# Optimization experiments

Hardware: AMD Instinct MI355X
Metric: run time of the kernel (lower is better)

Reference implementation:

```python
import jax, jax.numpy as jnp
import numpy as np

B, S, D, H, FF = 4, 2048, 512, 8, 2048
W = 128  # local attention window size (hardcoded in module)
DH = D // H


def _ln(x, g, b, eps=1e-5):
    m = x.mean(-1, keepdims=True)
    v = ((x - m) ** 2).mean(-1, keepdims=True)
    return (x - m) / jnp.sqrt(v + eps) * g + b


def setup_inputs() -> dict:
    key = jax.random.key(0)
    ks = jax.random.split(key, 10)
    s = 0.02
    return {
        "src": jax.random.normal(ks[0], (B, S, D), jnp.float32),
        # global nn.MultiheadAttention params
        "in_proj_w": jax.random.normal(ks[1], (3 * D, D), jnp.float32) * s,
        "in_proj_b": jnp.zeros((3 * D,), jnp.float32),
        "out_proj_w": jax.random.normal(ks[2], (D, D), jnp.float32) * s,
        "out_proj_b": jnp.zeros((D,), jnp.float32),
        # LocalMHA params (prenorm LN, fused qkv no-bias, out proj no-bias)
        "ln_g": jnp.ones((D,), jnp.float32),
        "ln_b": jnp.zeros((D,), jnp.float32),
        "qkv_w": jax.random.normal(ks[3], (3 * D, D), jnp.float32) * s,
        "to_out_w": jax.random.normal(ks[4], (D, D), jnp.float32) * s,
        # glFusion + FFN + norms
        "gl_w": jax.random.normal(ks[5], (D, 2 * D), jnp.float32) * s,
        "gl_b": jnp.zeros((D,), jnp.float32),
        "norm1_g": jnp.ones((D,), jnp.float32),
        "norm1_b": jnp.zeros((D,), jnp.float32),
        "lin1_w": jax.random.normal(ks[6], (FF, D), jnp.float32) * s,
        "lin1_b": jnp.zeros((FF,), jnp.float32),
        "lin2_w": jax.random.normal(ks[7], (D, FF), jnp.float32) * s,
        "lin2_b": jnp.zeros((D,), jnp.float32),
        "norm2_g": jnp.ones((D,), jnp.float32),
        "norm2_b": jnp.zeros((D,), jnp.float32),
    }


def _forward(src, in_proj_w, in_proj_b, out_proj_w, out_proj_b, ln_g, ln_b,
             qkv_w, to_out_w, gl_w, gl_b, norm1_g, norm1_b,
             lin1_w, lin1_b, lin2_w, lin2_b, norm2_g, norm2_b):
    b, s, d = src.shape
    scale = DH ** -0.5

    def heads(x):  # (b, s, d) -> (b, H, s, DH)
        return x.reshape(b, s, H, DH).transpose(0, 2, 1, 3)

    # ---- global full MHA (no mask) ----
    qkv = src @ in_proj_w.T + in_proj_b
    qg, kg, vg = (heads(t) for t in jnp.split(qkv, 3, axis=-1))
    att = jax.nn.softmax(jnp.einsum('bhid,bhjd->bhij', qg, kg) * scale, axis=-1)
    go = jnp.einsum('bhij,bhjd->bhid', att, vg).transpose(0, 2, 1, 3).reshape(b, s, d)
    go = go @ out_proj_w.T + out_proj_b

    # ---- local windowed causal MHA with rotary (window=128, look_backward=1) ----
    x = _ln(src, ln_g, ln_b)  # prenorm
    ql, kl, vl = (heads(t) for t in jnp.split(x @ qkv_w.T, 3, axis=-1))

    pos = jnp.arange(s)
    inv_freq = 1.0 / (10000.0 ** (jnp.arange(0, DH, 2, dtype=jnp.float32) / DH))
    freqs = pos[:, None].astype(jnp.float32) * inv_freq[None, :]
    emb = jnp.concatenate([freqs, freqs], axis=-1)  # (s, DH)
    cos, sin = jnp.cos(emb), jnp.sin(emb)

    def rope(t):
        h = DH // 2
        t1, t2 = t[..., :h], t[..., h:]
        return t * cos + jnp.concatenate([-t2, t1], axis=-1) * sin

    ql, kl = rope(ql), rope(kl)
    ql = ql * scale

    nw = s // W
    qw = ql.reshape(b, H, nw, W, DH)
    kw = kl.reshape(b, H, nw, W, DH)
    vw = vl.reshape(b, H, nw, W, DH)

    def look_back(t):  # concat previous window with current: (b,H,nw,2W,DH)
        prev = jnp.pad(t, ((0, 0), (0, 0), (1, 0), (0, 0), (0, 0)))[:, :, :-1]
        return jnp.concatenate([prev, t], axis=3)

    bk, bv = look_back(kw), look_back(vw)

    qpos = pos.reshape(nw, W)
    kpos = jnp.concatenate(
        [jnp.concatenate([jnp.full((1, W), -1, pos.dtype), qpos[:-1]], axis=0), qpos],
        axis=1)  # (nw, 2W)
    mask = (kpos[:, None, :] >= 0) & (kpos[:, None, :] <= qpos[:, :, None])  # (nw,W,2W)

    sc = jnp.einsum('bhnid,bhnjd->bhnij', qw, bk)
    sc = jnp.where(mask, sc, jnp.finfo(sc.dtype).min)
    at = jax.nn.softmax(sc, axis=-1)
    lo = jnp.einsum('bhnij,bhnjd->bhnid', at, bv).reshape(b, H, s, DH)
    lo = lo.transpose(0, 2, 1, 3).reshape(b, s, d) @ to_out_w.T

    # ---- fuse global+local, residual, norms, FFN ----
    src2 = jnp.concatenate([go, lo], axis=-1) @ gl_w.T + gl_b
    h1 = _ln(src + src2, norm1_g, norm1_b)
    ff = jax.nn.relu(h1 @ lin1_w.T + lin1_b) @ lin2_w.T + lin2_b
    return _ln(h1 + ff, norm2_g, norm2_b)


def reference(src, in_proj_w, in_proj_b, out_proj_w, out_proj_b, ln_g, ln_b,
              qkv_w, to_out_w, gl_w, gl_b, norm1_g, norm1_b,
              lin1_w, lin1_b, lin2_w, lin2_b, norm2_g, norm2_b):
    return _forward(src, in_proj_w, in_proj_b, out_proj_w, out_proj_b, ln_g, ln_b,
                    qkv_w, to_out_w, gl_w, gl_b, norm1_g, norm1_b,
                    lin1_w, lin1_b, lin2_w, lin2_b, norm2_g, norm2_b)
```

## Files before the change

kernel.cpp:

```cpp
#include <hip/hip_runtime.h>
#include <math.h>

#define B_  4
#define S_  2048
#define D_  512
#define H_  8
#define FF_ 2048
#define W_  128
#define DH_ 64
#define TRD (3*D_)
#define MR_ (B_*S_)
#define QKLD 1024
#define SCQ 0.18033688011112042f

typedef __attribute__((ext_vector_type(8)))  short short8;
typedef __attribute__((ext_vector_type(4)))  float f32x4;
typedef __attribute__((ext_vector_type(16))) float f32x16;

__device__ __forceinline__ short f2bf(float f) {
    unsigned u = __float_as_uint(f);
    unsigned r = (u + 0x7fff + ((u >> 16) & 1)) >> 16;
    return (short)r;
}
__device__ __forceinline__ float bf2f(ushort u) {
    return __uint_as_float(((unsigned)u) << 16);
}
__device__ __forceinline__ unsigned pack_bf_trunc(float f0, float f1) {
    return __builtin_amdgcn_perm(__float_as_uint(f1), __float_as_uint(f0), 0x07060302u);
}
__device__ __forceinline__ void gload_lds16(const ushort* g, short* l) {
    __builtin_amdgcn_global_load_lds(
        (const __attribute__((address_space(1))) void*)g,
        (__attribute__((address_space(3))) void*)l, 16, 0, 0);
}

struct CvtJobs { const float* s[8]; ushort* d[8]; int n[8]; };

__global__ __launch_bounds__(256) void cvt_kernel(CvtJobs jobs)
{
    int i4 = (blockIdx.x * 256 + threadIdx.x) * 4;
    #pragma unroll
    for (int j = 0; j < 8; j++) {
        if (i4 < jobs.n[j]) {
            float4 v = *(const float4*)(jobs.s[j] + i4);
            ushort4 o;
            o.x = (ushort)f2bf(v.x); o.y = (ushort)f2bf(v.y);
            o.z = (ushort)f2bf(v.z); o.w = (ushort)f2bf(v.w);
            *(ushort4*)(jobs.d[j] + i4) = o;
        }
    }
}

__global__ __launch_bounds__(256) void gemm_bf16_kernel(
    const ushort* __restrict__ A, int lda,
    const ushort* __restrict__ Wt,
    const float* __restrict__ bias,
    ushort* __restrict__ C, int ldc,
    ushort* __restrict__ vt,
    int K, int relu)
{
    __shared__ short As[128 * 64];
    __shared__ short Bs[128 * 64];
    const int tid  = threadIdx.x;
    const int w    = tid >> 6;
    const int lane = tid & 63;
    const int quad = lane >> 4;
    const int x    = lane & 15;
    const int wr = w >> 1, wc = w & 1;
    const int bm = blockIdx.y * 128;
    const int bn = blockIdx.x * 128;

    const int srow = w * 32 + (lane >> 3);
    const int scol = ((lane & 7) ^ (lane >> 3)) * 8;

    f32x4 acc[4][4];
    #pragma unroll
    for (int i = 0; i < 4; i++)
        #pragma unroll
        for (int j = 0; j < 4; j++) acc[i][j] = (f32x4)0.f;

    for (int k0 = 0; k0 < K; k0 += 64) {
        __syncthreads();
        #pragma unroll
        for (int c = 0; c < 4; c++) {
            const ushort* ga = A + (size_t)(bm + srow + c * 8) * lda + k0 + scol;
            gload_lds16(ga, &As[(w * 32 + c * 8) * 64]);
            const ushort* gb = Wt + (size_t)(bn + srow + c * 8) * K + k0 + scol;
            gload_lds16(gb, &Bs[(w * 32 + c * 8) * 64]);
        }
        __syncthreads();

        #pragma unroll
        for (int kc = 0; kc < 2; kc++) {
            short8 af[4], bf[4];
            int pcg = (kc * 4 + quad) ^ (x & 7);
            #pragma unroll
            for (int i = 0; i < 4; i++)
                af[i] = *(const short8*)&As[(wr * 64 + i * 16 + x) * 64 + pcg * 8];
            #pragma unroll
            for (int j = 0; j < 4; j++)
                bf[j] = *(const short8*)&Bs[(wc * 64 + j * 16 + x) * 64 + pcg * 8];
            #pragma unroll
            for (int i = 0; i < 4; i++)
                #pragma unroll
                for (int j = 0; j < 4; j++)
                    acc[i][j] = __builtin_amdgcn_mfma_f32_16x16x32_bf16(af[i], bf[j], acc[i][j], 0, 0, 0);
        }
    }

    if (vt) {
        #pragma unroll
        for (int i = 0; i < 4; i++) {
            int rowbase = bm + wr * 64 + i * 16 + quad * 4;
            #pragma unroll
            for (int j = 0; j < 4; j++) {
                int col = bn + wc * 64 + j * 16 + x;
                float bv = bias ? bias[col] : 0.f;
                if (col < 1024) {
                    #pragma unroll
                    for (int r = 0; r < 4; r++)
                        C[(size_t)(rowbase + r) * QKLD + col] = (ushort)f2bf(acc[i][j][r] + bv);
                } else {
                    int cv = col - 1024, hh = cv >> 6, dd = cv & 63;
                    int bb = rowbase >> 11, ss = rowbase & 2047;
                    int quadp = ((quad & 1) << 1) | (quad >> 1);
                    int sp = (ss & ~15) | (quadp << 2);
                    ushort4 p4;
                    p4.x = (ushort)f2bf(acc[i][j][0] + bv);
                    p4.y = (ushort)f2bf(acc[i][j][1] + bv);
                    p4.z = (ushort)f2bf(acc[i][j][2] + bv);
                    p4.w = (ushort)f2bf(acc[i][j][3] + bv);
                    *(ushort4*)(vt + ((size_t)((bb * 8 + hh) * 64 + dd)) * S_ + sp) = p4;
                }
            }
        }
    } else {
        #pragma unroll
        for (int i = 0; i < 4; i++) {
            #pragma unroll
            for (int r = 0; r < 4; r++) {
                size_t row = (size_t)(bm + wr * 64 + i * 16 + quad * 4 + r);
                #pragma unroll
                for (int j = 0; j < 4; j++) {
                    int col = bn + wc * 64 + j * 16 + x;
                    float v = acc[i][j][r] + (bias ? bias[col] : 0.f);
                    if (relu) v = v > 0.f ? v : 0.f;
                    C[row * ldc + col] = (ushort)f2bf(v);
                }
            }
        }
    }
}

__global__ __launch_bounds__(256) void gemm_bf16_splitk_kernel(
    const ushort* __restrict__ A, int lda,
    const ushort* __restrict__ Wt,
    float* __restrict__ P, int K)
{
    __shared__ short As[128 * 64];
    __shared__ short Bs[128 * 64];
    const int tid  = threadIdx.x;
    const int w    = tid >> 6;
    const int lane = tid & 63;
    const int quad = lane >> 4;
    const int x    = lane & 15;
    const int wr = w >> 1, wc = w & 1;
    const int bm = blockIdx.y * 128;
    const int bn = blockIdx.x * 128;
    const int kh = K >> 1;
    const int kbeg = blockIdx.z * kh;
    float* dst = P + (size_t)blockIdx.z * MR_ * D_;

    const int srow = w * 32 + (lane >> 3);
    const int scol = ((lane & 7) ^ (lane >> 3)) * 8;

    f32x4 acc[4][4];
    #pragma unroll
    for (int i = 0; i < 4; i++)
        #pragma unroll
        for (int j = 0; j < 4; j++) acc[i][j] = (f32x4)0.f;

    for (int k0 = kbeg; k0 < kbeg + kh; k0 += 64) {
        __syncthreads();
        #pragma unroll
        for (int c = 0; c < 4; c++) {
            const ushort* ga = A + (size_t)(bm + srow + c * 8) * lda + k0 + scol;
            gload_lds16(ga, &As[(w * 32 + c * 8) * 64]);
            const ushort* gb = Wt + (size_t)(bn + srow + c * 8) * K + k0 + scol;
            gload_lds16(gb, &Bs[(w * 32 + c * 8) * 64]);
        }
        __syncthreads();

        #pragma unroll
        for (int kc = 0; kc < 2; kc++) {
            short8 af[4], bf[4];
            int pcg = (kc * 4 + quad) ^ (x & 7);
            #pragma unroll
            for (int i = 0; i < 4; i++)
                af[i] = *(const short8*)&As[(wr * 64 + i * 16 + x) * 64 + pcg * 8];
            #pragma unroll
            for (int j = 0; j < 4; j++)
                bf[j] = *(const short8*)&Bs[(wc * 64 + j * 16 + x) * 64 + pcg * 8];
            #pragma unroll
            for (int i = 0; i < 4; i++)
                #pragma unroll
                for (int j = 0; j < 4; j++)
                    acc[i][j] = __builtin_amdgcn_mfma_f32_16x16x32_bf16(af[i], bf[j], acc[i][j], 0, 0, 0);
        }
    }

    #pragma unroll
    for (int i = 0; i < 4; i++)
        #pragma unroll
        for (int r = 0; r < 4; r++) {
            size_t row = (size_t)(bm + wr * 64 + i * 16 + quad * 4 + r);
            #pragma unroll
            for (int j = 0; j < 4; j++) {
                int col = bn + wc * 64 + j * 16 + x;
                dst[row * D_ + col] = acc[i][j][r];
            }
        }
}

__device__ __forceinline__ float wave_sum64(float v) {
    #pragma unroll
    for (int off = 32; off > 0; off >>= 1) v += __shfl_xor(v, off, 64);
    return v;
}
__device__ __forceinline__ void load8(const float* p, float* v) {
    *(float4*)&v[0] = *(const float4*)p;
    *(float4*)&v[4] = *(const float4*)(p + 4);
}
__device__ __forceinline__ void load8(const ushort* p, float* v) {
    short8 s = *(const short8*)p;
    #pragma unroll
    for (int i = 0; i < 8; i++) v[i] = bf2f((ushort)s[i]);
}
__device__ __forceinline__ void store8(float* p, const float* v) {
    *(float4*)p       = make_float4(v[0], v[1], v[2], v[3]);
    *(float4*)(p + 4) = make_float4(v[4], v[5], v[6], v[7]);
}
__device__ __forceinline__ void store8(ushort* p, const float* v) {
    short8 s;
    #pragma unroll
    for (int i = 0; i < 8; i++) s[i] = f2bf(v[i]);
    *(short8*)p = s;
}
__device__ __forceinline__ void ln_core(float* v, int lane,
    const float* g, const float* be, float* t) {
    float s = 0.f;
    #pragma unroll
    for (int i = 0; i < 8; i++) s += v[i];
    float mean = wave_sum64(s) * (1.0f / 512.0f);
    float vs = 0.f;
    #pragma unroll
    for (int i = 0; i < 8; i++) { float d = v[i] - mean; vs += d * d; }
    float var = wave_sum64(vs) * (1.0f / 512.0f);
    float r = rsqrtf(var + 1e-5f);
    const int c = lane * 8;
    #pragma unroll
    for (int i = 0; i < 8; i++) t[i] = (v[i] - mean) * r * g[c + i] + be[c + i];
}

template <typename TA, typename TO>
__global__ __launch_bounds__(256) void addln_kernel(
    const TA* __restrict__ a,
    const float* __restrict__ g, const float* __restrict__ be,
    TO* __restrict__ out)
{
    const int lane = threadIdx.x & 63;
    const int row  = blockIdx.x * 4 + (threadIdx.x >> 6);
    const size_t base = (size_t)row * D_ + lane * 8;
    float v[8], t[8];
    load8(a + base, v);
    ln_core(v, lane, g, be, t);
    store8(out + base, t);
}

template <typename TA, typename TO>
__global__ __launch_bounds__(256) void ln_split_kernel(
    const TA* __restrict__ a,
    const float* __restrict__ p0, const float* __restrict__ p1,
    const float* __restrict__ bias,
    const float* __restrict__ g, const float* __restrict__ be,
    TO* __restrict__ out)
{
    const int lane = threadIdx.x & 63;
    const int row  = blockIdx.x * 4 + (threadIdx.x >> 6);
    const size_t base = (size_t)row * D_ + lane * 8;
    float v[8], w0[8], w1[8], t[8];
    load8(a + base, v);
    load8(p0 + base, w0);
    load8(p1 + base, w1);
    const int c = lane * 8;
    #pragma unroll
    for (int i = 0; i < 8; i++) v[i] += w0[i] + w1[i] + bias[c + i];
    ln_core(v, lane, g, be, t);
    store8(out + base, t);
}

__global__ __launch_bounds__(256) void transpose512_kernel(
    const ushort* __restrict__ in, ushort* __restrict__ out)
{
    __shared__ ushort T[64][72];
    const int t  = threadIdx.x;
    const int r0 = blockIdx.y * 64, c0 = blockIdx.x * 64;
    {
        int row = t >> 2, col = (t & 3) * 16;
        const ushort* s = in + (size_t)(r0 + row) * 512 + c0 + col;
        *(short8*)&T[row][col]     = *(const short8*)s;
        *(short8*)&T[row][col + 8] = *(const short8*)(s + 8);
    }
    __syncthreads();
    {
        int d = t >> 2, sc = (t & 3) * 16;
        ushort tmp[16];
        #pragma unroll
        for (int k = 0; k < 16; k++) tmp[k] = T[sc + k][d];
        ushort* dptr = out + (size_t)(c0 + d) * 512 + r0 + sc;
        *(short8*)dptr       = *(const short8*)&tmp[0];
        *(short8*)(dptr + 8) = *(const short8*)&tmp[8];
    }
}

__global__ __launch_bounds__(256) void fuse_bias_kernel(
    const float* __restrict__ gl_w, const float* __restrict__ opb,
    const float* __restrict__ gl_b, float* __restrict__ bf)
{
    const int lane = threadIdx.x & 63;
    const int row  = blockIdx.x * 4 + (threadIdx.x >> 6);
    float s = 0.f;
    #pragma unroll
    for (int i = 0; i < 8; i++) {
        int m = lane * 8 + i;
        s += gl_w[(size_t)row * 1024 + m] * opb[m];
    }
    s = wave_sum64(s);
    if (lane == 0) bf[row] = s + gl_b[row];
}

__global__ __launch_bounds__(256) void rope_kernel(ushort* __restrict__ qk)
{
    int idx = blockIdx.x * 256 + threadIdx.x;
    int d8 = idx & 3;
    int h  = (idx >> 2) & 7;
    int bs = idx >> 5;
    int pos = bs & (S_ - 1);
    ushort* base = qk + (size_t)bs * QKLD + h * 64 + d8 * 8;
    float q1[8], q2[8], k1[8], k2[8];
    load8(base, q1);       load8(base + 32, q2);
    load8(base + 512, k1); load8(base + 544, k2);
    float oq1[8], oq2[8], ok1[8], ok2[8];
    #pragma unroll
    for (int i = 0; i < 8; i++) {
        int d = d8 * 8 + i;
        float inv_freq = exp2f(-(float)d * (2.0f / 64.0f) * 13.287712379549449f);
        float ang = (float)pos * inv_freq;
        float sn, cs;
        __sincosf(ang, &sn, &cs);
        oq1[i] = (q1[i] * cs - q2[i] * sn) * SCQ;
        oq2[i] = (q2[i] * cs + q1[i] * sn) * SCQ;
        ok1[i] = k1[i] * cs - k2[i] * sn;
        ok2[i] = k2[i] * cs + k1[i] * sn;
    }
    store8(base, oq1);       store8(base + 32, oq2);
    store8(base + 512, ok1); store8(base + 544, ok2);
}

__global__ __launch_bounds__(256) void attn_kernel(
    const ushort* __restrict__ qkG, const ushort* __restrict__ vtG,
    const ushort* __restrict__ qkL, const ushort* __restrict__ vtL,
    ushort* __restrict__ cat)
{
    __shared__ short KsS[2][64 * 64];
    __shared__ short VtS[2][64 * 64];
    __shared__ float Lw[4][32];

    const int LOCAL = blockIdx.z;
    const ushort* qk = LOCAL ? qkL : qkG;
    const ushort* vt = LOCAL ? vtL : vtG;
    ushort* outp = cat + (LOCAL ? D_ : 0);

    const int tid  = threadIdx.x;
    const int w    = tid >> 6;
    const int lane = tid & 63;
    const int hl   = lane >> 5;
    const int c    = lane & 31;
    const int ks   = w >> 1;
    const int qh   = w & 1;
    const int bh = blockIdx.y;
    const int b = bh >> 3, h = bh & 7;
    const int qbase = blockIdx.x * 64;
    const int q0 = qbase + qh * 32;
    const size_t bS = (size_t)b * S_;
    const size_t vbase = (size_t)bh * DH_;

    short8 aq[4];
    {
        const ushort* qp = qk + (bS + q0 + c) * QKLD + h * 64;
        #pragma unroll
        for (int kc = 0; kc < 4; kc++) {
            short8 raw = *(const short8*)(qp + kc * 16 + hl * 8);
            if (LOCAL) aq[kc] = raw;
            else {
                #pragma unroll
                for (int j = 0; j < 8; j++) aq[kc][j] = f2bf(bf2f((ushort)raw[j]) * SCQ);
            }
        }
    }

    f32x16 ot[2];
    ot[0] = (f32x16)0.f; ot[1] = (f32x16)0.f;
    float lpa = 0.f, lpb = 0.f;

    const int rowk = qh * 32 + (lane >> 3);
    const int cg   = (lane & 7) ^ (lane >> 3);
    short* ldsk = &KsS[ks][(qh * 32) * 64];
    short* ldsv = &VtS[ks][(qh * 32) * 64];

    if (!LOCAL) {
        const ushort* gk = qk + (bS + ks * 1024 + rowk) * QKLD + 512 + h * 64 + cg * 8;
        const ushort* gv = vt + (vbase + rowk) * S_ + ks * 1024 + cg * 8;
        for (int it = 0; it < 16; it++) {
            __syncthreads();
            #pragma unroll
            for (int cc = 0; cc < 4; cc++) {
                gload_lds16(gk + (size_t)(cc * 8) * QKLD, ldsk + cc * 8 * 64);
                gload_lds16(gv + (size_t)(cc * 8) * S_,   ldsv + cc * 8 * 64);
            }
            __syncthreads();
            gk += 64 * QKLD;
            gv += 64;

            f32x16 e0 = (f32x16)0.f, e1 = (f32x16)0.f;
            #pragma unroll
            for (int kc = 0; kc < 4; kc++) {
                int pcg = (kc * 2 + hl) ^ (c & 7);
                short8 ak0 = *(const short8*)&KsS[ks][c * 64 + pcg * 8];
                e0 = __builtin_amdgcn_mfma_f32_32x32x16_bf16(ak0, aq[kc], e0, 0, 0, 0);
                short8 ak1 = *(const short8*)&KsS[ks][(32 + c) * 64 + pcg * 8];
                e1 = __builtin_amdgcn_mfma_f32_32x32x16_bf16(ak1, aq[kc], e1, 0, 0, 0);
            }
            #pragma unroll
            for (int r = 0; r < 16; r++) { e0[r] = exp2f(e0[r]); }
            #pragma unroll
            for (int r = 0; r < 16; r++) { e1[r] = exp2f(e1[r]); }
            #pragma unroll
            for (int r = 0; r < 8; r++) {
                lpa += e0[2 * r] + e1[2 * r];
                lpb += e0[2 * r + 1] + e1[2 * r + 1];
            }
            #pragma unroll
            for (int t = 0; t < 4; t++) {
                const f32x16& e = (t < 2) ? e0 : e1;
                const int rb = 8 * (t & 1);
                uint4 u;
                u.x = pack_bf_trunc(e[rb + 0], e[rb + 1]);
                u.y = pack_bf_trunc(e[rb + 2], e[rb + 3]);
                u.z = pack_bf_trunc(e[rb + 4], e[rb + 5]);
                u.w = pack_bf_trunc(e[rb + 6], e[rb + 7]);
                short8 bp = *(short8*)&u;
                #pragma unroll
                for (int dt = 0; dt < 2; dt++) {
                    int row = dt * 32 + c;
                    int pcg = (t * 2 + hl) ^ (c & 7);
                    short8 av = *(const short8*)&VtS[ks][row * 64 + pcg * 8];
                    ot[dt] = __builtin_amdgcn_mfma_f32_32x32x16_bf16(av, bp, ot[dt], 0, 0, 0);
                }
            }
        }
    } else {
        for (int it = 0; it < 2; it++) {
            const int tile  = ks * 2 + it;
            const int kbase = (qbase >> 7) * 128 - 128 + tile * 64;
            const bool active = (kbase >= 0 && kbase <= qbase + 63);
            __syncthreads();
            if (active) {
                #pragma unroll
                for (int cc = 0; cc < 4; cc++) {
                    gload_lds16(qk + (bS + kbase + rowk + cc * 8) * QKLD + 512 + h * 64 + cg * 8,
                                ldsk + cc * 8 * 64);
                    gload_lds16(vt + (vbase + rowk + cc * 8) * S_ + kbase + cg * 8,
                                ldsv + cc * 8 * 64);
                }
            }
            __syncthreads();
            if (!active) continue;
            const bool diag = (kbase == qbase);

            f32x16 e0 = (f32x16)0.f, e1 = (f32x16)0.f;
            #pragma unroll
            for (int kc = 0; kc < 4; kc++) {
                int pcg = (kc * 2 + hl) ^ (c & 7);
                short8 ak0 = *(const short8*)&KsS[ks][c * 64 + pcg * 8];
                e0 = __builtin_amdgcn_mfma_f32_32x32x16_bf16(ak0, aq[kc], e0, 0, 0, 0);
                short8 ak1 = *(const short8*)&KsS[ks][(32 + c) * 64 + pcg * 8];
                e1 = __builtin_amdgcn_mfma_f32_32x32x16_bf16(ak1, aq[kc], e1, 0, 0, 0);
            }
            const int qi = q0 + c;
            #pragma unroll
            for (int mt = 0; mt < 2; mt++) {
                f32x16& e = mt ? e1 : e0;
                #pragma unroll
                for (int r = 0; r < 16; r++) {
                    float p = exp2f(e[r]);
                    if (diag) {
                        int key = kbase + mt * 32 + (r & 3) + 8 * (r >> 2) + 4 * hl;
                        if (key > qi) p = 0.f;
                    }
                    e[r] = p;
                }
            }
            #pragma unroll
            for (int r = 0; r < 8; r++) {
                lpa += e0[2 * r] + e1[2 * r];
                lpb += e0[2 * r + 1] + e1[2 * r + 1];
            }
            #pragma unroll
            for (int t = 0; t < 4; t++) {
                const f32x16& e = (t < 2) ? e0 : e1;
                const int rb = 8 * (t & 1);
                uint4 u;
                u.x = pack_bf_trunc(e[rb + 0], e[rb + 1]);
                u.y = pack_bf_trunc(e[rb + 2], e[rb + 3]);
                u.z = pack_bf_trunc(e[rb + 4], e[rb + 5]);
                u.w = pack_bf_trunc(e[rb + 6], e[rb + 7]);
                short8 bp = *(short8*)&u;
                #pragma unroll
                for (int dt = 0; dt < 2; dt++) {
                    int row = dt * 32 + c;
                    int pcg = (t * 2 + hl) ^ (c & 7);
                    short8 av = *(const short8*)&VtS[ks][row * 64 + pcg * 8];
                    ot[dt] = __builtin_amdgcn_mfma_f32_32x32x16_bf16(av, bp, ot[dt], 0, 0, 0);
                }
            }
        }
    }

    float lp = lpa + lpb;
    lp += __shfl_xor(lp, 32, 64);
    if (hl == 0) Lw[w][c] = lp;
    __syncthreads();

    float* scr = (float*)&KsS[0][0];
    if (w >= 2) {
        float* dst = scr + (w - 2) * 2048;
        #pragma unroll
        for (int dt = 0; dt < 2; dt++)
            #pragma unroll
            for (int r = 0; r < 16; r++)
                dst[(dt * 16 + r) * 64 + lane] = ot[dt][r];
    }
    __syncthreads();
    if (w < 2) {
        const float* srcp = scr + w * 2048;
        #pragma unroll
        for (int dt = 0; dt < 2; dt++)
            #pragma unroll
            for (int r = 0; r < 16; r++)
                ot[dt][r] += srcp[(dt * 16 + r) * 64 + lane];
        float inv = 1.0f / (Lw[w][c] + Lw[w + 2][c]);

        short* tr = (short*)&VtS[0][0] + w * 2304;
        #pragma unroll
        for (int dt = 0; dt < 2; dt++)
            #pragma unroll
            for (int rq = 0; rq < 4; rq++) {
                uint2 pkv;
                pkv.x = pack_bf_trunc(ot[dt][rq * 4 + 0] * inv, ot[dt][rq * 4 + 1] * inv);
                pkv.y = pack_bf_trunc(ot[dt][rq * 4 + 2] * inv, ot[dt][rq * 4 + 3] * inv);
                *(uint2*)&tr[c * 72 + dt * 32 + 8 * rq + 4 * hl] = pkv;
            }
        asm volatile("s_waitcnt lgkmcnt(0)" ::: "memory");
        __builtin_amdgcn_wave_barrier();
        {
            int q  = lane >> 1;
            int d0 = (lane & 1) * 32;
            short8 v0 = *(const short8*)&tr[q * 72 + d0];
            short8 v1 = *(const short8*)&tr[q * 72 + d0 + 8];
            short8 v2 = *(const short8*)&tr[q * 72 + d0 + 16];
            short8 v3 = *(const short8*)&tr[q * 72 + d0 + 24];
            ushort* op = outp + (bS + q0 + q) * 1024 + h * 64 + d0;
            *(short8*)(op)      = v0;
            *(short8*)(op + 8)  = v1;
            *(short8*)(op + 16) = v2;
            *(short8*)(op + 24) = v3;
        }
    }
}

extern "C" void kernel_launch(void* const* d_in, const int* in_sizes, int n_in,
                              void* d_out, int out_size, void* d_ws, size_t ws_size,
                              hipStream_t stream)
{
    (void)in_sizes; (void)n_in; (void)out_size; (void)ws_size;
    const float* src        = (const float*)d_in[0];
    const float* in_proj_w  = (const float*)d_in[1];
    const float* in_proj_b  = (const float*)d_in[2];
    const float* out_proj_w = (const float*)d_in[3];
    const float* out_proj_b = (const float*)d_in[4];
    const float* ln_g       = (const float*)d_in[5];
    const float* ln_b       = (const float*)d_in[6];
    const float* qkv_w      = (const float*)d_in[7];
    const float* to_out_w   = (const float*)d_in[8];
    const float* gl_w       = (const float*)d_in[9];
    const float* gl_b       = (const float*)d_in[10];
    const float* norm1_g    = (const float*)d_in[11];
    const float* norm1_b    = (const float*)d_in[12];
    const float* lin1_w     = (const float*)d_in[13];
    const float* lin1_b     = (const float*)d_in[14];
    const float* lin2_w     = (const float*)d_in[15];
    const float* lin2_b     = (const float*)d_in[16];
    const float* norm2_g    = (const float*)d_in[17];
    const float* norm2_b    = (const float*)d_in[18];
    float* out = (float*)d_out;

    ushort* ws16   = (ushort*)d_ws;
    ushort* src_bf = ws16;
    ushort* wi_bf  = src_bf + (size_t)MR_ * D_;
    ushort* wq_bf  = wi_bf  + TRD * D_;
    ushort* wo_bf  = wq_bf  + TRD * D_;
    ushort* wt_bf  = wo_bf  + D_ * D_;
    ushort* wg_bf  = wt_bf  + D_ * D_;
    ushort* w1_bf  = wg_bf  + D_ * 2 * D_;
    ushort* w2_bf  = w1_bf  + FF_ * D_;
    ushort* opwT   = w2_bf  + D_ * FF_;
    ushort* towT   = opwT   + D_ * D_;
    ushort* wcat   = towT   + D_ * D_;
    float*  bfuse  = (float*)(wcat + D_ * 2 * D_);
    ushort* buf1   = (ushort*)(bfuse + D_);
    ushort* h1b    = buf1 + (size_t)MR_ * D_;
    ushort* qkG    = h1b  + (size_t)MR_ * D_;
    ushort* vtg    = qkG  + (size_t)MR_ * QKLD;
    ushort* qkL    = vtg  + (size_t)MR_ * D_;
    ushort* vtl    = qkL  + (size_t)MR_ * QKLD;
    ushort* cat    = vtl  + (size_t)MR_ * D_;
    float*  part   = (float*)qkG;
    ushort* ff1    = qkL + (size_t)MR_ * D_;

    dim3 blk256(256);

    CvtJobs jobs;
    jobs.s[0] = src;        jobs.d[0] = src_bf; jobs.n[0] = MR_ * D_;
    jobs.s[1] = in_proj_w;  jobs.d[1] = wi_bf;  jobs.n[1] = TRD * D_;
    jobs.s[2] = qkv_w;      jobs.d[2] = wq_bf;  jobs.n[2] = TRD * D_;
    jobs.s[3] = out_proj_w; jobs.d[3] = wo_bf;  jobs.n[3] = D_ * D_;
    jobs.s[4] = to_out_w;   jobs.d[4] = wt_bf;  jobs.n[4] = D_ * D_;
    jobs.s[5] = gl_w;       jobs.d[5] = wg_bf;  jobs.n[5] = D_ * 2 * D_;
    jobs.s[6] = lin1_w;     jobs.d[6] = w1_bf;  jobs.n[6] = FF_ * D_;
    jobs.s[7] = lin2_w;     jobs.d[7] = w2_bf;  jobs.n[7] = D_ * FF_;
    cvt_kernel<<<dim3(4096), blk256, 0, stream>>>(jobs);

    transpose512_kernel<<<dim3(8, 8), blk256, 0, stream>>>(wo_bf, opwT);
    transpose512_kernel<<<dim3(8, 8), blk256, 0, stream>>>(wt_bf, towT);
    gemm_bf16_kernel<<<dim3(4, 4), blk256, 0, stream>>>(
        wg_bf, 2 * D_, opwT, nullptr, wcat, 2 * D_, nullptr, D_, 0);
    gemm_bf16_kernel<<<dim3(4, 4), blk256, 0, stream>>>(
        wg_bf + D_, 2 * D_, towT, nullptr, wcat + D_, 2 * D_, nullptr, D_, 0);
    fuse_bias_kernel<<<dim3(D_ / 4), blk256, 0, stream>>>(gl_w, out_proj_b, gl_b, bfuse);

    gemm_bf16_kernel<<<dim3(TRD / 128, MR_ / 128), blk256, 0, stream>>>(
        src_bf, D_, wi_bf, in_proj_b, qkG, QKLD, vtg, D_, 0);
    addln_kernel<float, ushort><<<dim3(MR_ / 4), blk256, 0, stream>>>(
        src, ln_g, ln_b, buf1);
    gemm_bf16_kernel<<<dim3(TRD / 128, MR_ / 128), blk256, 0, stream>>>(
        buf1, D_, wq_bf, nullptr, qkL, QKLD, vtl, D_, 0);
    rope_kernel<<<dim3((B_ * S_ * H_ * 4) / 256), blk256, 0, stream>>>(qkL);
    attn_kernel<<<dim3(S_ / 64, B_ * H_, 2), blk256, 0, stream>>>(
        qkG, vtg, qkL, vtl, cat);
    gemm_bf16_splitk_kernel<<<dim3(D_ / 128, MR_ / 128, 2), blk256, 0, stream>>>(
        cat, 2 * D_, wcat, part, 2 * D_);
    ln_split_kernel<float, ushort><<<dim3(MR_ / 4), blk256, 0, stream>>>(
        src, part, part + (size_t)MR_ * D_, bfuse, norm1_g, norm1_b, h1b);
    gemm_bf16_kernel<<<dim3(FF_ / 128, MR_ / 128), blk256, 0, stream>>>(
        h1b, D_, w1_bf, lin1_b, ff1, FF_, nullptr, D_, 1);
    gemm_bf16_splitk_kernel<<<dim3(D_ / 128, MR_ / 128, 2), blk256, 0, stream>>>(
        ff1, FF_, w2_bf, part, FF_);
    ln_split_kernel<ushort, float><<<dim3(MR_ / 4), blk256, 0, stream>>>(
        h1b, part, part + (size_t)MR_ * D_, lin2_b, norm2_g, norm2_b, out);
}
```

Measured before the change: 412.7 us.

## Restructure attention to 128-query blocks and move V transpose to separate kernel

Attention blocks now cover 128 queries with each wave owning 32 queries over the full key range. This removes the split-key partial-output reduction through LDS and halves the number of K/V tile loads per query. The V transpose is no longer done with scattered stores in the QKV GEMM epilogue; the GEMM writes V row-major and a new LDS transpose kernel produces the permuted V^T layout. This adds two extra kernel launches and an extra pass over V. Attention now launches half as many blocks, which lowers parallelism.

After: 429.2 us. 4.0% more time.

```diff
diff --git a/kernel.cpp b/kernel.cpp
--- a/kernel.cpp
+++ b/kernel.cpp
@@ -56,7 +56,7 @@
     const ushort* __restrict__ Wt,
     const float* __restrict__ bias,
     ushort* __restrict__ C, int ldc,
-    ushort* __restrict__ vt,
+    ushort* __restrict__ vbuf,
     int K, int relu)
 {
     __shared__ short As[128 * 64];
@@ -108,29 +108,18 @@
         }
     }
 
-    if (vt) {
+    if (vbuf) {
         #pragma unroll
         for (int i = 0; i < 4; i++) {
-            int rowbase = bm + wr * 64 + i * 16 + quad * 4;
-            #pragma unroll
-            for (int j = 0; j < 4; j++) {
-                int col = bn + wc * 64 + j * 16 + x;
-                float bv = bias ? bias[col] : 0.f;
-                if (col < 1024) {
-                    #pragma unroll
-                    for (int r = 0; r < 4; r++)
-                        C[(size_t)(rowbase + r) * QKLD + col] = (ushort)f2bf(acc[i][j][r] + bv);
-                } else {
-                    int cv = col - 1024, hh = cv >> 6, dd = cv & 63;
-                    int bb = rowbase >> 11, ss = rowbase & 2047;
-                    int quadp = ((quad & 1) << 1) | (quad >> 1);
-                    int sp = (ss & ~15) | (quadp << 2);
-                    ushort4 p4;
-                    p4.x = (ushort)f2bf(acc[i][j][0] + bv);
-                    p4.y = (ushort)f2bf(acc[i][j][1] + bv);
-                    p4.z = (ushort)f2bf(acc[i][j][2] + bv);
-                    p4.w = (ushort)f2bf(acc[i][j][3] + bv);
-                    *(ushort4*)(vt + ((size_t)((bb * 8 + hh) * 64 + dd)) * S_ + sp) = p4;
+            #pragma unroll
+            for (int r = 0; r < 4; r++) {
+                size_t row = (size_t)(bm + wr * 64 + i * 16 + quad * 4 + r);
+                #pragma unroll
+                for (int j = 0; j < 4; j++) {
+                    int col = bn + wc * 64 + j * 16 + x;
+                    float v = acc[i][j][r] + (bias ? bias[col] : 0.f);
+                    if (col < 1024) C[row * QKLD + col] = (ushort)f2bf(v);
+                    else            vbuf[row * 512 + (col - 1024)] = (ushort)f2bf(v);
                 }
             }
         }
@@ -323,6 +312,35 @@
     }
 }
 
+__global__ __launch_bounds__(256) void transpose_vp_kernel(
+    const ushort* __restrict__ vb, ushort* __restrict__ vt)
+{
+    __shared__ ushort T[64][72];
+    const int t  = threadIdx.x;
+    const int s0 = blockIdx.x * 64;
+    const int bh = blockIdx.y;
+    const int b = bh >> 3, h = bh & 7;
+    {
+        int row = t >> 2, col = (t & 3) * 16;
+        const ushort* s = vb + ((size_t)(b * S_) + s0 + row) * 512 + h * 64 + col;
+        *(short8*)&T[row][col]     = *(const short8*)s;
+        *(short8*)&T[row][col + 8] = *(const short8*)(s + 8);
+    }
+    __syncthreads();
+    {
+        int d = t >> 2, sc = (t & 3) * 16;
+        ushort tmp[16];
+        #pragma unroll
+        for (int k = 0; k < 16; k++) {
+            int sk = (k & 3) | ((k & 4) << 1) | ((k & 8) >> 1);
+            tmp[k] = T[sc + sk][d];
+        }
+        ushort* dptr = vt + ((size_t)bh * DH_ + d) * S_ + s0 + sc;
+        *(short8*)dptr       = *(const short8*)&tmp[0];
+        *(short8*)(dptr + 8) = *(const short8*)&tmp[8];
+    }
+}
+
 __global__ __launch_bounds__(256) void fuse_bias_kernel(
     const float* __restrict__ gl_w, const float* __restrict__ opb,
     const float* __restrict__ gl_b, float* __restrict__ bf)
@@ -372,9 +390,9 @@
     const ushort* __restrict__ qkL, const ushort* __restrict__ vtL,
     ushort* __restrict__ cat)
 {
-    __shared__ short KsS[2][64 * 64];
-    __shared__ short VtS[2][64 * 64];
-    __shared__ float Lw[4][32];
+    __shared__ short SMEM[10240];
+    short* Ks = SMEM;
+    short* Vt = SMEM + 4096;
 
     const int LOCAL = blockIdx.z;
     const ushort* qk = LOCAL ? qkL : qkG;
@@ -386,12 +404,10 @@
     const int lane = tid & 63;
     const int hl   = lane >> 5;
     const int c    = lane & 31;
-    const int ks   = w >> 1;
-    const int qh   = w & 1;
     const int bh = blockIdx.y;
     const int b = bh >> 3, h = bh & 7;
-    const int qbase = blockIdx.x * 64;
-    const int q0 = qbase + qh * 32;
+    const int qbase = blockIdx.x * 128;
+    const int q0 = qbase + w * 32;
     const size_t bS = (size_t)b * S_;
     const size_t vbase = (size_t)bh * DH_;
 
@@ -413,18 +429,18 @@
     ot[0] = (f32x16)0.f; ot[1] = (f32x16)0.f;
     float lpa = 0.f, lpb = 0.f;
 
-    const int rowk = qh * 32 + (lane >> 3);
+    const int rowk = w * 16 + (lane >> 3);
     const int cg   = (lane & 7) ^ (lane >> 3);
-    short* ldsk = &KsS[ks][(qh * 32) * 64];
-    short* ldsv = &VtS[ks][(qh * 32) * 64];
+    short* ldsk = Ks + (w * 16) * 64;
+    short* ldsv = Vt + (w * 16) * 64;
 
     if (!LOCAL) {
-        const ushort* gk = qk + (bS + ks * 1024 + rowk) * QKLD + 512 + h * 64 + cg * 8;
-        const ushort* gv = vt + (vbase + rowk) * S_ + ks * 1024 + cg * 8;
-        for (int it = 0; it < 16; it++) {
+        const ushort* gk = qk + (bS + rowk) * QKLD + 512 + h * 64 + cg * 8;
+        const ushort* gv = vt + (vbase + rowk) * S_ + cg * 8;
+        for (int it = 0; it < 32; it++) {
             __syncthreads();
             #pragma unroll
-            for (int cc = 0; cc < 4; cc++) {
+            for (int cc = 0; cc < 2; cc++) {
                 gload_lds16(gk + (size_t)(cc * 8) * QKLD, ldsk + cc * 8 * 64);
                 gload_lds16(gv + (size_t)(cc * 8) * S_,   ldsv + cc * 8 * 64);
             }
@@ -436,9 +452,9 @@
             #pragma unroll
             for (int kc = 0; kc < 4; kc++) {
                 int pcg = (kc * 2 + hl) ^ (c & 7);
-                short8 ak0 = *(const short8*)&KsS[ks][c * 64 + pcg * 8];
+                short8 ak0 = *(const short8*)&Ks[c * 64 + pcg * 8];
                 e0 = __builtin_amdgcn_mfma_f32_32x32x16_bf16(ak0, aq[kc], e0, 0, 0, 0);
-                short8 ak1 = *(const short8*)&KsS[ks][(32 + c) * 64 + pcg * 8];
+                short8 ak1 = *(const short8*)&Ks[(32 + c) * 64 + pcg * 8];
                 e1 = __builtin_amdgcn_mfma_f32_32x32x16_bf16(ak1, aq[kc], e1, 0, 0, 0);
             }
             #pragma unroll
@@ -464,20 +480,19 @@
                 for (int dt = 0; dt < 2; dt++) {
                     int row = dt * 32 + c;
                     int pcg = (t * 2 + hl) ^ (c & 7);
-                    short8 av = *(const short8*)&VtS[ks][row * 64 + pcg * 8];
+                    short8 av = *(const short8*)&Vt[row * 64 + pcg * 8];
                     ot[dt] = __builtin_amdgcn_mfma_f32_32x32x16_bf16(av, bp, ot[dt], 0, 0, 0);
                 }
             }
         }
     } else {
-        for (int it = 0; it < 2; it++) {
-            const int tile  = ks * 2 + it;
-            const int kbase = (qbase >> 7) * 128 - 128 + tile * 64;
-            const bool active = (kbase >= 0 && kbase <= qbase + 63);
+        for (int it = 0; it < 4; it++) {
+            const int kbase = qbase - 128 + it * 64;
+            const bool activeB = (kbase >= 0);
             __syncthreads();
-            if (active) {
-                #pragma unroll
-                for (int cc = 0; cc < 4; cc++) {
+            if (activeB) {
+                #pragma unroll
+                for (int cc = 0; cc < 2; cc++) {
                     gload_lds16(qk + (bS + kbase + rowk + cc * 8) * QKLD + 512 + h * 64 + cg * 8,
                                 ldsk + cc * 8 * 64);
                     gload_lds16(vt + (vbase + rowk + cc * 8) * S_ + kbase + cg * 8,
@@ -485,16 +500,17 @@
                 }
             }
             __syncthreads();
-            if (!active) continue;
-            const bool diag = (kbase == qbase);
+            if (!activeB) continue;
+            if (kbase >= q0 + 32) continue;
+            const bool needmask = (kbase + 63 > q0);
 
             f32x16 e0 = (f32x16)0.f, e1 = (f32x16)0.f;
             #pragma unroll
             for (int kc = 0; kc < 4; kc++) {
                 int pcg = (kc * 2 + hl) ^ (c & 7);
-                short8 ak0 = *(const short8*)&KsS[ks][c * 64 + pcg * 8];
+                short8 ak0 = *(const short8*)&Ks[c * 64 + pcg * 8];
                 e0 = __builtin_amdgcn_mfma_f32_32x32x16_bf16(ak0, aq[kc], e0, 0, 0, 0);
-                short8 ak1 = *(const short8*)&KsS[ks][(32 + c) * 64 + pcg * 8];
+                short8 ak1 = *(const short8*)&Ks[(32 + c) * 64 + pcg * 8];
                 e1 = __builtin_amdgcn_mfma_f32_32x32x16_bf16(ak1, aq[kc], e1, 0, 0, 0);
             }
             const int qi = q0 + c;
@@ -504,7 +520,7 @@
                 #pragma unroll
                 for (int r = 0; r < 16; r++) {
                     float p = exp2f(e[r]);
-                    if (diag) {
+                    if (needmask) {
                         int key = kbase + mt * 32 + (r & 3) + 8 * (r >> 2) + 4 * hl;
                         if (key > qi) p = 0.f;
                     }
@@ -530,7 +546,7 @@
                 for (int dt = 0; dt < 2; dt++) {
                     int row = dt * 32 + c;
                     int pcg = (t * 2 + hl) ^ (c & 7);
-                    short8 av = *(const short8*)&VtS[ks][row * 64 + pcg * 8];
+                    short8 av = *(const short8*)&Vt[row * 64 + pcg * 8];
                     ot[dt] = __builtin_amdgcn_mfma_f32_32x32x16_bf16(av, bp, ot[dt], 0, 0, 0);
                 }
             }
@@ -539,53 +555,33 @@
 
     float lp = lpa + lpb;
     lp += __shfl_xor(lp, 32, 64);
-    if (hl == 0) Lw[w][c] = lp;
+    float inv = 1.0f / lp;
+
     __syncthreads();
-
-    float* scr = (float*)&KsS[0][0];
-    if (w >= 2) {
-        float* dst = scr + (w - 2) * 2048;
-        #pragma unroll
-        for (int dt = 0; dt < 2; dt++)
-            #pragma unroll
-            for (int r = 0; r < 16; r++)
-                dst[(dt * 16 + r) * 64 + lane] = ot[dt][r];
-    }
-    __syncthreads();
-    if (w < 2) {
-        const float* srcp = scr + w * 2048;
-        #pragma unroll
-        for (int dt = 0; dt < 2; dt++)
-            #pragma unroll
-            for (int r = 0; r < 16; r++)
-                ot[dt][r] += srcp[(dt * 16 + r) * 64 + lane];
-        float inv = 1.0f / (Lw[w][c] + Lw[w + 2][c]);
-
-        short* tr = (short*)&VtS[0][0] + w * 2304;
-        #pragma unroll
-        for (int dt = 0; dt < 2; dt++)
-            #pragma unroll
-            for (int rq = 0; rq < 4; rq++) {
-                uint2 pkv;
-                pkv.x = pack_bf_trunc(ot[dt][rq * 4 + 0] * inv, ot[dt][rq * 4 + 1] * inv);
-                pkv.y = pack_bf_trunc(ot[dt][rq * 4 + 2] * inv, ot[dt][rq * 4 + 3] * inv);
-                *(uint2*)&tr[c * 72 + dt * 32 + 8 * rq + 4 * hl] = pkv;
-            }
-        asm volatile("s_waitcnt lgkmcnt(0)" ::: "memory");
-        __builtin_amdgcn_wave_barrier();
-        {
-            int q  = lane >> 1;
-            int d0 = (lane & 1) * 32;
-            short8 v0 = *(const short8*)&tr[q * 72 + d0];
-            short8 v1 = *(const short8*)&tr[q * 72 + d0 + 8];
-            short8 v2 = *(const short8*)&tr[q * 72 + d0 + 16];
-            short8 v3 = *(const short8*)&tr[q * 72 + d0 + 24];
-            ushort* op = outp + (bS + q0 + q) * 1024 + h * 64 + d0;
-            *(short8*)(op)      = v0;
-            *(short8*)(op + 8)  = v1;
-            *(short8*)(op + 16) = v2;
-            *(short8*)(op + 24) = v3;
-        }
+    short* tr = SMEM + w * 2304;
+    #pragma unroll
+    for (int dt = 0; dt < 2; dt++)
+        #pragma unroll
+        for (int rq = 0; rq < 4; rq++) {
+            uint2 pkv;
+            pkv.x = pack_bf_trunc(ot[dt][rq * 4 + 0] * inv, ot[dt][rq * 4 + 1] * inv);
+            pkv.y = pack_bf_trunc(ot[dt][rq * 4 + 2] * inv, ot[dt][rq * 4 + 3] * inv);
+            *(uint2*)&tr[c * 72 + dt * 32 + 8 * rq + 4 * hl] = pkv;
+        }
+    asm volatile("s_waitcnt lgkmcnt(0)" ::: "memory");
+    __builtin_amdgcn_wave_barrier();
+    {
+        int q  = lane >> 1;
+        int d0 = (lane & 1) * 32;
+        short8 v0 = *(const short8*)&tr[q * 72 + d0];
+        short8 v1 = *(const short8*)&tr[q * 72 + d0 + 8];
+        short8 v2 = *(const short8*)&tr[q * 72 + d0 + 16];
+        short8 v3 = *(const short8*)&tr[q * 72 + d0 + 24];
+        ushort* op = outp + (bS + q0 + q) * 1024 + h * 64 + d0;
+        *(short8*)(op)      = v0;
+        *(short8*)(op + 8)  = v1;
+        *(short8*)(op + 16) = v2;
+        *(short8*)(op + 24) = v3;
     }
 }
 
@@ -635,6 +631,8 @@
     ushort* qkL    = vtg  + (size_t)MR_ * D_;
     ushort* vtl    = qkL  + (size_t)MR_ * QKLD;
     ushort* cat    = vtl  + (size_t)MR_ * D_;
+    ushort* vbufG  = cat;
+    ushort* vbufL  = cat + (size_t)MR_ * D_;
     float*  part   = (float*)qkG;
     ushort* ff1    = qkL + (size_t)MR_ * D_;
 
@@ -660,13 +658,15 @@
     fuse_bias_kernel<<<dim3(D_ / 4), blk256, 0, stream>>>(gl_w, out_proj_b, gl_b, bfuse);
 
     gemm_bf16_kernel<<<dim3(TRD / 128, MR_ / 128), blk256, 0, stream>>>(
-        src_bf, D_, wi_bf, in_proj_b, qkG, QKLD, vtg, D_, 0);
+        src_bf, D_, wi_bf, in_proj_b, qkG, QKLD, vbufG, D_, 0);
+    transpose_vp_kernel<<<dim3(S_ / 64, B_ * H_), blk256, 0, stream>>>(vbufG, vtg);
     addln_kernel<float, ushort><<<dim3(MR_ / 4), blk256, 0, stream>>>(
         src, ln_g, ln_b, buf1);
     gemm_bf16_kernel<<<dim3(TRD / 128, MR_ / 128), blk256, 0, stream>>>(
-        buf1, D_, wq_bf, nullptr, qkL, QKLD, vtl, D_, 0);
+        buf1, D_, wq_bf, nullptr, qkL, QKLD, vbufL, D_, 0);
+    transpose_vp_kernel<<<dim3(S_ / 64, B_ * H_), blk256, 0, stream>>>(vbufL, vtl);
     rope_kernel<<<dim3((B_ * S_ * H_ * 4) / 256), blk256, 0, stream>>>(qkL);
-    attn_kernel<<<dim3(S_ / 64, B_ * H_, 2), blk256, 0, stream>>>(
+    attn_kernel<<<dim3(S_ / 128, B_ * H_, 2), blk256, 0, stream>>>(
         qkG, vtg, qkL, vtl, cat);
     gemm_bf16_splitk_kernel<<<dim3(D_ / 128, MR_ / 128, 2), blk256, 0, stream>>>(
         cat, 2 * D_, wcat, part, 2 * D_);
```
